# Kernel optimization log

Measured on AMD Instinct MI355X. Metric: run time of the kernel, lower is better.

Reference implementation:

```python
import jax, jax.numpy as jnp
import numpy as np

D_IN = 768
D_OUT = 768
NUM_HEADS = 12
HEAD_DIM = D_OUT // NUM_HEADS


def setup_inputs() -> dict:
    key = jax.random.key(0)
    ks = jax.random.split(key, 9)
    s = 1.0 / np.sqrt(D_IN)
    x = jax.random.normal(ks[0], (8, 1024, D_IN), dtype=jnp.float32)
    Wq = jax.random.uniform(ks[1], (D_IN, D_OUT), jnp.float32, -s, s)
    Wk = jax.random.uniform(ks[2], (D_IN, D_OUT), jnp.float32, -s, s)
    Wv = jax.random.uniform(ks[3], (D_IN, D_OUT), jnp.float32, -s, s)
    Wo = jax.random.uniform(ks[4], (D_OUT, D_OUT), jnp.float32, -s, s)
    bq = jax.random.uniform(ks[5], (D_OUT,), jnp.float32, -s, s)
    bk = jax.random.uniform(ks[6], (D_OUT,), jnp.float32, -s, s)
    bv = jax.random.uniform(ks[7], (D_OUT,), jnp.float32, -s, s)
    bo = jax.random.uniform(ks[8], (D_OUT,), jnp.float32, -s, s)
    return {"x": x, "Wq": Wq, "bq": bq, "Wk": Wk, "bk": bk,
            "Wv": Wv, "bv": bv, "Wo": Wo, "bo": bo}


def reference(x, Wq, bq, Wk, bk, Wv, bv, Wo, bo):
    b, n, _ = x.shape
    # projections -> (b, heads, n, head_dim)
    def split_heads(t):
        return t.reshape(b, n, NUM_HEADS, HEAD_DIM).transpose(0, 2, 1, 3)
    q = split_heads(x @ Wq + bq)
    k = split_heads(x @ Wk + bk)
    v = split_heads(x @ Wv + bv)
    scale = 1.0 / jnp.sqrt(jnp.float32(HEAD_DIM)).astype(x.dtype)
    scores = jnp.einsum('bhqd,bhkd->bhqk', q, k) * scale
    attn = jax.nn.softmax(scores, axis=-1)  # dropout p=0.0 -> identity
    ctx = jnp.einsum('bhqk,bhkd->bhqd', attn, v)
    ctx = ctx.transpose(0, 2, 1, 3).reshape(b, n, D_OUT)
    return ctx @ Wo + bo
```

## Files before the change

### kernel.cpp

```cpp
#include <hip/hip_runtime.h>
#include <math.h>

#define D_MODEL 768
#define NHEAD  12
#define HDIM   64
#define SEQ    1024
#define BATCH  8
#define MTOT   (BATCH*SEQ)
#define QKV_LD 2304

typedef _Float16 f16;
typedef __attribute__((ext_vector_type(2))) __fp16 fp16x2;
typedef __attribute__((ext_vector_type(4))) _Float16 f16x4;
typedef __attribute__((ext_vector_type(8))) _Float16 f16x8;
typedef __attribute__((ext_vector_type(4))) float f32x4;
typedef __attribute__((ext_vector_type(16))) float f32x16;

union PFrag { unsigned u[4]; f16x8 v; };
union PackW { fp16x2 h; unsigned u; };

__device__ inline void gload_lds16(const void* g, void* l) {
    __builtin_amdgcn_global_load_lds(
        (const __attribute__((address_space(1))) void*)g,
        (__attribute__((address_space(3))) void*)l, 16, 0, 0);
}

__global__ __launch_bounds__(256) void cvt_f32_f16(
    const float* __restrict__ in, f16* __restrict__ out, int n8)
{
    const int i = blockIdx.x * 256 + threadIdx.x;
    if (i < n8) {
        const float4 a = *(const float4*)(in + (size_t)i * 8);
        const float4 b = *(const float4*)(in + (size_t)i * 8 + 4);
        f16x8 v;
        v[0] = (f16)a.x; v[1] = (f16)a.y; v[2] = (f16)a.z; v[3] = (f16)a.w;
        v[4] = (f16)b.x; v[5] = (f16)b.y; v[6] = (f16)b.z; v[7] = (f16)b.w;
        *(f16x8*)(out + (size_t)i * 8) = v;
    }
}

__global__ __launch_bounds__(256) void concat_bias(
    const float* __restrict__ bq, const float* __restrict__ bk,
    const float* __restrict__ bv, float* __restrict__ bqkv)
{
    const int i = blockIdx.x * 256 + threadIdx.x;
    if (i < QKV_LD)
        bqkv[i] = (i < 768) ? bq[i] : (i < 1536) ? bk[i - 768] : bv[i - 1536];
}

__global__ __launch_bounds__(256) void transpose_cvt_all(
    const float* __restrict__ Wq, const float* __restrict__ Wk,
    const float* __restrict__ Wv, const float* __restrict__ Wo,
    f16* __restrict__ Wqkv_t, f16* __restrict__ Wo_t)
{
    const int z = blockIdx.z;
    const float* src = (z == 0) ? Wq : (z == 1) ? Wk : (z == 2) ? Wv : Wo;
    f16* dst = (z < 3) ? (Wqkv_t + (size_t)z * 768 * 768) : Wo_t;

    __shared__ f16 tile[64][72];
    const int t  = threadIdx.x;
    const int k0 = blockIdx.y * 64;
    const int n0 = blockIdx.x * 64;
    {
        const int r  = t >> 4;
        const int c4 = (t & 15) * 4;
        #pragma unroll
        for (int u = 0; u < 4; ++u) {
            const int row = r + u * 16;
            const float4 a = *(const float4*)&src[(size_t)(k0 + row) * 768 + n0 + c4];
            tile[row][c4 + 0] = (f16)a.x;
            tile[row][c4 + 1] = (f16)a.y;
            tile[row][c4 + 2] = (f16)a.z;
            tile[row][c4 + 3] = (f16)a.w;
        }
    }
    __syncthreads();
    {
        const int rn = t >> 3;
        const int ck = (t & 7) * 8;
        #pragma unroll
        for (int u = 0; u < 2; ++u) {
            const int n = rn + u * 32;
            f16x8 v;
            #pragma unroll
            for (int q = 0; q < 8; ++q) v[q] = tile[ck + q][n];
            *(f16x8*)&dst[(size_t)(n0 + n) * 768 + k0 + ck] = v;
        }
    }
}

template<typename OUT_T>
__global__ __launch_bounds__(256) void gemm_f16_tn(
    const f16* __restrict__ A, const f16* __restrict__ Bt,
    const float* __restrict__ bias, OUT_T* __restrict__ C,
    int M, int N, int K, int nb)
{
    __shared__ f16 As[128 * 32];
    __shared__ f16 Bs[128 * 32];

    const int t    = threadIdx.x;
    const int l    = t & 63;
    const int w    = t >> 6;
    const int l15  = l & 15;
    const int lg   = l >> 4;
    const int wrow = (w >> 1) * 64;
    const int wcol = (w & 1) * 64;

    const int orig = blockIdx.x;
    const int cpx  = gridDim.x >> 3;
    const int nid  = (orig & 7) * cpx + (orig >> 3);
    const int row0 = (nid / nb) * 128;
    const int col0 = (nid % nb) * 128;

    int src_row[2], src_koff[2], lds_off[2];
    #pragma unroll
    for (int i = 0; i < 2; ++i) {
        const int c = t + 256 * i;
        const int r = c >> 2;
        src_row[i]  = r;
        src_koff[i] = (((c & 3) - (r >> 1)) & 3) * 8;
        lds_off[i]  = c * 16;
    }

    int a_off[4], b_off[4];
    #pragma unroll
    for (int i = 0; i < 4; ++i) {
        const int ra = wrow + i * 16 + l15;
        a_off[i] = ra * 64 + (((lg + (ra >> 1)) & 3) * 16);
        const int rb = wcol + i * 16 + l15;
        b_off[i] = rb * 64 + (((lg + (rb >> 1)) & 3) * 16);
    }

    f32x4 acc[4][4];
    #pragma unroll
    for (int i = 0; i < 4; ++i)
        #pragma unroll
        for (int j = 0; j < 4; ++j)
            acc[i][j] = (f32x4){0.f, 0.f, 0.f, 0.f};

    const f16* Abase = A  + (size_t)row0 * K;
    const f16* Bbase = Bt + (size_t)col0 * K;

    for (int k0 = 0; k0 < K; k0 += 32) {
        #pragma unroll
        for (int i = 0; i < 2; ++i) {
            gload_lds16(Abase + (size_t)src_row[i] * K + k0 + src_koff[i],
                        (char*)As + lds_off[i]);
            gload_lds16(Bbase + (size_t)src_row[i] * K + k0 + src_koff[i],
                        (char*)Bs + lds_off[i]);
        }
        __syncthreads();

        f16x8 af[4], bf[4];
        #pragma unroll
        for (int i = 0; i < 4; ++i) {
            af[i] = *(const f16x8*)((const char*)As + a_off[i]);
            bf[i] = *(const f16x8*)((const char*)Bs + b_off[i]);
        }
        #pragma unroll
        for (int i = 0; i < 4; ++i)
            #pragma unroll
            for (int j = 0; j < 4; ++j)
                acc[i][j] = __builtin_amdgcn_mfma_f32_16x16x32_f16(
                    af[i], bf[j], acc[i][j], 0, 0, 0);
        __syncthreads();
    }

    #pragma unroll
    for (int j = 0; j < 4; ++j) {
        const int col = col0 + wcol + j * 16 + l15;
        const float bj = bias[col];
        #pragma unroll
        for (int i = 0; i < 4; ++i) {
            const int row = row0 + wrow + i * 16 + lg * 4;
            #pragma unroll
            for (int q = 0; q < 4; ++q)
                C[(size_t)(row + q) * N + col] = (OUT_T)(acc[i][j][q] + bj);
        }
    }
}

#define RESCALE_THR 10.0f
#define QMAP(r, hh) (((r) & 3) + 8 * ((r) >> 2) + 4 * (hh))

__global__ __launch_bounds__(256, 3) void attn_f16(
    const f16* __restrict__ QKV, f16* __restrict__ O)
{
    __shared__ f16 KsB[2][64 * 64];
    __shared__ f16 VtB[2][64 * 64];

    const int t   = threadIdx.x;
    const int w   = t >> 6;
    const int l   = t & 63;
    const int l31 = l & 31;
    const int h   = l >> 5;
    const int sl  = (l & 7) << 4;

    const int orig = blockIdx.x;
    const int s    = (orig & 7) * 96 + (orig >> 3);
    const int bh   = s >> 3;
    const int qb   = s & 7;
    const int b  = bh / NHEAD;
    const int hd = bh % NHEAD;
    const int q0 = qb * 128;

    const size_t rowbase = (size_t)b * SEQ;
    const int qcol = hd * HDIM;
    const int kcol = 768 + hd * HDIM;
    const int vcol = 1536 + hd * HDIM;

    const f16 hsc = (f16)(0.125f * 1.4426950408889634f);
    f16x8 qf[4];
    #pragma unroll
    for (int dc = 0; dc < 4; ++dc) {
        f16x8 v = *(const f16x8*)(QKV
            + (rowbase + q0 + w * 32 + l31) * QKV_LD
            + qcol + dc * 16 + h * 8);
        #pragma unroll
        for (int j = 0; j < 8; ++j) v[j] *= hsc;
        qf[dc] = v;
    }

    f32x16 ctx[2];
    #pragma unroll
    for (int dt = 0; dt < 2; ++dt)
        #pragma unroll
        for (int r = 0; r < 16; ++r) ctx[dt][r] = 0.f;
    float mrun = -INFINITY;
    float lrun = 0.f;

    const int cb  = w * 16;
    const int vk0 = (l & 15) * 4;
    const int vd0 = ((l >> 4) + 4 * w) * 4;
    const f16* kptr = QKV + (rowbase + l)   * QKV_LD + kcol + cb;
    const f16* vptr = QKV + (rowbase + vk0) * QKV_LD + vcol + vd0;
    const size_t step = (size_t)64 * QKV_LD;

    f16x8 kr0, kr1;
    f16x4 vr[4];
    kr0 = *(const f16x8*)(kptr);
    kr1 = *(const f16x8*)(kptr + 8);
    #pragma unroll
    for (int i = 0; i < 4; ++i)
        vr[i] = *(const f16x4*)(vptr + (size_t)i * QKV_LD);

    {
        char* Kd = (char*)KsB[0];
        char* Vd = (char*)VtB[0];
        *(f16x8*)(Kd + l * 128 + ((cb * 2)      ^ sl)) = kr0;
        *(f16x8*)(Kd + l * 128 + ((cb * 2 + 16) ^ sl)) = kr1;
        #pragma unroll
        for (int di = 0; di < 4; ++di) {
            f16x4 wt;
            #pragma unroll
            for (int i = 0; i < 4; ++i) wt[i] = vr[i][di];
            *(f16x4*)(Vd + (vd0 + di) * 128
                         + ((vk0 * 2) ^ (((vd0 + di) & 7) << 4))) = wt;
        }
    }
    kr0 = *(const f16x8*)(kptr + step);
    kr1 = *(const f16x8*)(kptr + step + 8);
    #pragma unroll
    for (int i = 0; i < 4; ++i)
        vr[i] = *(const f16x4*)(vptr + step + (size_t)i * QKV_LD);
    __syncthreads();

    for (int kt = 0; kt < SEQ / 64; ++kt) {
        const int p = kt & 1;
        const char* Kp = (const char*)KsB[p];
        const char* Vp = (const char*)VtB[p];

        f32x16 sacc[2];
        __builtin_amdgcn_s_setprio(1);
        #pragma unroll
        for (int kk = 0; kk < 2; ++kk) {
            f32x16 a;
            #pragma unroll
            for (int r = 0; r < 16; ++r) a[r] = 0.f;
            #pragma unroll
            for (int dc = 0; dc < 4; ++dc) {
                const f16x8 ka = *(const f16x8*)(Kp + (kk * 32 + l31) * 128
                                                    + ((dc * 32 + h * 16) ^ sl));
                a = __builtin_amdgcn_mfma_f32_32x32x16_f16(ka, qf[dc], a, 0, 0, 0);
            }
            sacc[kk] = a;
        }
        __builtin_amdgcn_s_setprio(0);

        {
            float tmax = sacc[0][0];
            #pragma unroll
            for (int r = 1; r < 16; ++r) tmax = fmaxf(tmax, sacc[0][r]);
            #pragma unroll
            for (int r = 0; r < 16; ++r) tmax = fmaxf(tmax, sacc[1][r]);
            tmax = fmaxf(tmax, __shfl_xor(tmax, 32));

            if (__any(tmax > mrun + RESCALE_THR)) {
                const float mnew = fmaxf(mrun, tmax);
                const float corr = exp2f(mrun - mnew);
                mrun = mnew;
                lrun *= corr;
                #pragma unroll
                for (int r = 0; r < 16; ++r) {
                    const float cr = __shfl(corr, QMAP(r, h));
                    ctx[0][r] *= cr;
                    ctx[1][r] *= cr;
                }
            }

            float ps = 0.f;
            #pragma unroll
            for (int kk = 0; kk < 2; ++kk)
                #pragma unroll
                for (int r = 0; r < 16; ++r) {
                    const float pe = exp2f(sacc[kk][r] - mrun);
                    ps += pe;
                    sacc[kk][r] = pe;
                }
            ps += __shfl_xor(ps, 32);
            lrun += ps;
        }

        unsigned paw[4][4];
        #pragma unroll
        for (int kk = 0; kk < 2; ++kk) {
            unsigned dw[8];
            #pragma unroll
            for (int i = 0; i < 8; ++i) {
                PackW u;
                u.h = __builtin_amdgcn_cvt_pkrtz(sacc[kk][2 * i], sacc[kk][2 * i + 1]);
                dw[i] = u.u;
            }
            const unsigned t0 = (unsigned)__shfl_xor((int)(h ? dw[0] : dw[2]), 32);
            const unsigned t1 = (unsigned)__shfl_xor((int)(h ? dw[1] : dw[3]), 32);
            const unsigned t2 = (unsigned)__shfl_xor((int)(h ? dw[4] : dw[6]), 32);
            const unsigned t3 = (unsigned)__shfl_xor((int)(h ? dw[5] : dw[7]), 32);
            paw[2 * kk][0]     = h ? t0    : dw[0];
            paw[2 * kk][1]     = h ? t1    : dw[1];
            paw[2 * kk][2]     = h ? dw[2] : t0;
            paw[2 * kk][3]     = h ? dw[3] : t1;
            paw[2 * kk + 1][0] = h ? t2    : dw[4];
            paw[2 * kk + 1][1] = h ? t3    : dw[5];
            paw[2 * kk + 1][2] = h ? dw[6] : t2;
            paw[2 * kk + 1][3] = h ? dw[7] : t3;
        }

        __builtin_amdgcn_s_setprio(1);
        #pragma unroll
        for (int c = 0; c < 4; ++c) {
            PFrag pf;
            pf.u[0] = paw[c][0]; pf.u[1] = paw[c][1];
            pf.u[2] = paw[c][2]; pf.u[3] = paw[c][3];
            #pragma unroll
            for (int dt = 0; dt < 2; ++dt) {
                const f16x8 vb = *(const f16x8*)(Vp + (dt * 32 + l31) * 128
                                                    + ((c * 32 + h * 16) ^ sl));
                ctx[dt] = __builtin_amdgcn_mfma_f32_32x32x16_f16(pf.v, vb, ctx[dt], 0, 0, 0);
            }
        }
        __builtin_amdgcn_s_setprio(0);

        if (kt < SEQ / 64 - 1) {
            char* Kd = (char*)KsB[p ^ 1];
            char* Vd = (char*)VtB[p ^ 1];
            *(f16x8*)(Kd + l * 128 + ((cb * 2)      ^ sl)) = kr0;
            *(f16x8*)(Kd + l * 128 + ((cb * 2 + 16) ^ sl)) = kr1;
            #pragma unroll
            for (int di = 0; di < 4; ++di) {
                f16x4 wt;
                #pragma unroll
                for (int i = 0; i < 4; ++i) wt[i] = vr[i][di];
                *(f16x4*)(Vd + (vd0 + di) * 128
                             + ((vk0 * 2) ^ (((vd0 + di) & 7) << 4))) = wt;
            }
            if (kt < SEQ / 64 - 2) {
                const f16* kp = kptr + (size_t)(kt + 2) * step;
                const f16* vp = vptr + (size_t)(kt + 2) * step;
                kr0 = *(const f16x8*)(kp);
                kr1 = *(const f16x8*)(kp + 8);
                #pragma unroll
                for (int i = 0; i < 4; ++i)
                    vr[i] = *(const f16x4*)(vp + (size_t)i * QKV_LD);
            }
        }
        __syncthreads();
    }

    {
        const float inv = 1.0f / lrun;
        #pragma unroll
        for (int r = 0; r < 16; ++r) {
            const float iv = __shfl(inv, QMAP(r, h));
            const size_t row = rowbase + q0 + w * 32 + QMAP(r, h);
            O[row * D_MODEL + qcol + l31]      = (f16)(ctx[0][r] * iv);
            O[row * D_MODEL + qcol + 32 + l31] = (f16)(ctx[1][r] * iv);
        }
    }
}

extern "C" void kernel_launch(void* const* d_in, const int* in_sizes, int n_in,
                              void* d_out, int out_size, void* d_ws, size_t ws_size,
                              hipStream_t stream) {
    const float* x  = (const float*)d_in[0];
    const float* Wq = (const float*)d_in[1];
    const float* bq = (const float*)d_in[2];
    const float* Wk = (const float*)d_in[3];
    const float* bk = (const float*)d_in[4];
    const float* Wv = (const float*)d_in[5];
    const float* bv = (const float*)d_in[6];
    const float* Wo = (const float*)d_in[7];
    const float* bo = (const float*)d_in[8];
    float* out = (float*)d_out;

    char* ws = (char*)d_ws;
    f16*   QKV     = (f16*)(ws);
    f16*   xh      = (f16*)(ws + 37748736);
    f16*   ctxh    = (f16*)(ws + 37748736 + 12582912);
    f16*   Wqkv_t  = (f16*)(ws + 37748736 + 2 * 12582912);
    f16*   Wo_t    = (f16*)(ws + 37748736 + 2 * 12582912 + 3538944);
    float* bqkv    = (float*)(ws + 37748736 + 2 * 12582912 + 3538944 + 1179648);

    hipLaunchKernelGGL(cvt_f32_f16, dim3(MTOT * D_MODEL / 8 / 256), dim3(256), 0, stream,
                       x, xh, MTOT * D_MODEL / 8);
    hipLaunchKernelGGL(concat_bias, dim3(9), dim3(256), 0, stream, bq, bk, bv, bqkv);
    hipLaunchKernelGGL(transpose_cvt_all, dim3(12, 12, 4), dim3(256), 0, stream,
                       Wq, Wk, Wv, Wo, Wqkv_t, Wo_t);

    hipLaunchKernelGGL((gemm_f16_tn<f16>), dim3((QKV_LD / 128) * (MTOT / 128)), dim3(256), 0, stream,
                       xh, Wqkv_t, bqkv, QKV, MTOT, QKV_LD, D_MODEL, QKV_LD / 128);

    hipLaunchKernelGGL(attn_f16, dim3((SEQ / 128) * BATCH * NHEAD), dim3(256), 0, stream,
                       QKV, ctxh);

    hipLaunchKernelGGL((gemm_f16_tn<float>), dim3((D_MODEL / 128) * (MTOT / 128)), dim3(256), 0, stream,
                       ctxh, Wo_t, bo, out, MTOT, D_MODEL, D_MODEL, D_MODEL / 128);
}
```

Baseline: 139.8 us.

## Split KV sequence across wave pairs in attention and merge partial softmax states

The attention kernel now processes 64 query rows per block instead of 128, doubling the grid. The four waves form two pairs, each pair handling half of the key/value sequence (8 tiles each) with its own single-buffered shared-memory tiles. Partial (max, sum, context) states are merged through shared memory at the end, and occupancy is raised to 4 blocks per CU. Row max and sum reductions are also rewritten as tree reductions. The aim is more parallelism and shorter per-block serial loops, at the cost of an extra merge step, an extra barrier per iteration, and no double buffering.

```diff
diff --git a/kernel.cpp b/kernel.cpp
--- a/kernel.cpp
+++ b/kernel.cpp
@@ -183,38 +183,42 @@
 #define RESCALE_THR 10.0f
 #define QMAP(r, hh) (((r) & 3) + 8 * ((r) >> 2) + 4 * (hh))
 
-__global__ __launch_bounds__(256, 3) void attn_f16(
+__global__ __launch_bounds__(256, 4) void attn_f16(
     const f16* __restrict__ QKV, f16* __restrict__ O)
 {
-    __shared__ f16 KsB[2][64 * 64];
-    __shared__ f16 VtB[2][64 * 64];
+    __shared__ __align__(16) char smem[32768];
 
     const int t   = threadIdx.x;
     const int w   = t >> 6;
     const int l   = t & 63;
     const int l31 = l & 31;
     const int h   = l >> 5;
+    const int g   = w >> 1;
+    const int sh  = w & 1;
     const int sl  = (l & 7) << 4;
 
     const int orig = blockIdx.x;
-    const int s    = (orig & 7) * 96 + (orig >> 3);
-    const int bh   = s >> 3;
-    const int qb   = s & 7;
+    const int s    = (orig & 7) * 192 + (orig >> 3);
+    const int bh   = s >> 4;
+    const int qb   = s & 15;
     const int b  = bh / NHEAD;
     const int hd = bh % NHEAD;
-    const int q0 = qb * 128;
+    const int q0 = qb * 64;
 
     const size_t rowbase = (size_t)b * SEQ;
     const int qcol = hd * HDIM;
     const int kcol = 768 + hd * HDIM;
     const int vcol = 1536 + hd * HDIM;
 
+    char* Ksh = smem + sh * 8192;
+    char* Vsh = smem + 16384 + sh * 8192;
+
     const f16 hsc = (f16)(0.125f * 1.4426950408889634f);
     f16x8 qf[4];
     #pragma unroll
     for (int dc = 0; dc < 4; ++dc) {
         f16x8 v = *(const f16x8*)(QKV
-            + (rowbase + q0 + w * 32 + l31) * QKV_LD
+            + (rowbase + q0 + g * 32 + l31) * QKV_LD
             + qcol + dc * 16 + h * 8);
         #pragma unroll
         for (int j = 0; j < 8; ++j) v[j] *= hsc;
@@ -229,47 +233,40 @@
     float mrun = -INFINITY;
     float lrun = 0.f;
 
-    const int cb  = w * 16;
+    const int kc0 = g * 32;
     const int vk0 = (l & 15) * 4;
-    const int vd0 = ((l >> 4) + 4 * w) * 4;
-    const f16* kptr = QKV + (rowbase + l)   * QKV_LD + kcol + cb;
+    const int vd0 = (l >> 4) * 8 + g * 32;
+    const f16* kptr = QKV + (rowbase + l)   * QKV_LD + kcol + kc0;
     const f16* vptr = QKV + (rowbase + vk0) * QKV_LD + vcol + vd0;
     const size_t step = (size_t)64 * QKV_LD;
-
-    f16x8 kr0, kr1;
-    f16x4 vr[4];
-    kr0 = *(const f16x8*)(kptr);
-    kr1 = *(const f16x8*)(kptr + 8);
-    #pragma unroll
-    for (int i = 0; i < 4; ++i)
-        vr[i] = *(const f16x4*)(vptr + (size_t)i * QKV_LD);
-
-    {
-        char* Kd = (char*)KsB[0];
-        char* Vd = (char*)VtB[0];
-        *(f16x8*)(Kd + l * 128 + ((cb * 2)      ^ sl)) = kr0;
-        *(f16x8*)(Kd + l * 128 + ((cb * 2 + 16) ^ sl)) = kr1;
-        #pragma unroll
-        for (int di = 0; di < 4; ++di) {
-            f16x4 wt;
-            #pragma unroll
-            for (int i = 0; i < 4; ++i) wt[i] = vr[i][di];
-            *(f16x4*)(Vd + (vd0 + di) * 128
-                         + ((vk0 * 2) ^ (((vd0 + di) & 7) << 4))) = wt;
-        }
-    }
-    kr0 = *(const f16x8*)(kptr + step);
-    kr1 = *(const f16x8*)(kptr + step + 8);
-    #pragma unroll
-    for (int i = 0; i < 4; ++i)
-        vr[i] = *(const f16x4*)(vptr + step + (size_t)i * QKV_LD);
+    const size_t tb   = (size_t)(sh * 8) * step;
+
+    f16x8 kr[4], vr[4];
+    #pragma unroll
+    for (int j = 0; j < 4; ++j) {
+        kr[j] = *(const f16x8*)(kptr + tb + j * 8);
+        vr[j] = *(const f16x8*)(vptr + tb + (size_t)j * QKV_LD);
+    }
+
+    #pragma unroll
+    for (int j = 0; j < 4; ++j)
+        *(f16x8*)(Ksh + l * 128 + (((kc0 + j * 8) * 2) ^ sl)) = kr[j];
+    #pragma unroll
+    for (int dj = 0; dj < 8; ++dj) {
+        f16x4 wt;
+        #pragma unroll
+        for (int i = 0; i < 4; ++i) wt[i] = vr[i][dj];
+        *(f16x4*)(Vsh + (vd0 + dj) * 128
+                     + ((vk0 * 2) ^ (((vd0 + dj) & 7) << 4))) = wt;
+    }
+    #pragma unroll
+    for (int j = 0; j < 4; ++j) {
+        kr[j] = *(const f16x8*)(kptr + tb + step + j * 8);
+        vr[j] = *(const f16x8*)(vptr + tb + step + (size_t)j * QKV_LD);
+    }
     __syncthreads();
 
-    for (int kt = 0; kt < SEQ / 64; ++kt) {
-        const int p = kt & 1;
-        const char* Kp = (const char*)KsB[p];
-        const char* Vp = (const char*)VtB[p];
-
+    for (int it = 0; it < 8; ++it) {
         f32x16 sacc[2];
         __builtin_amdgcn_s_setprio(1);
         #pragma unroll
@@ -279,8 +276,8 @@
             for (int r = 0; r < 16; ++r) a[r] = 0.f;
             #pragma unroll
             for (int dc = 0; dc < 4; ++dc) {
-                const f16x8 ka = *(const f16x8*)(Kp + (kk * 32 + l31) * 128
-                                                    + ((dc * 32 + h * 16) ^ sl));
+                const f16x8 ka = *(const f16x8*)(Ksh + (kk * 32 + l31) * 128
+                                                     + ((dc * 32 + h * 16) ^ sl));
                 a = __builtin_amdgcn_mfma_f32_32x32x16_f16(ka, qf[dc], a, 0, 0, 0);
             }
             sacc[kk] = a;
@@ -288,12 +285,16 @@
         __builtin_amdgcn_s_setprio(0);
 
         {
-            float tmax = sacc[0][0];
-            #pragma unroll
-            for (int r = 1; r < 16; ++r) tmax = fmaxf(tmax, sacc[0][r]);
-            #pragma unroll
-            for (int r = 0; r < 16; ++r) tmax = fmaxf(tmax, sacc[1][r]);
-            tmax = fmaxf(tmax, __shfl_xor(tmax, 32));
+            float tm[16];
+            #pragma unroll
+            for (int r = 0; r < 16; ++r)
+                tm[r] = fmaxf(sacc[0][r], sacc[1][r]);
+            #pragma unroll
+            for (int off = 8; off >= 1; off >>= 1)
+                #pragma unroll
+                for (int r = 0; r < 8; ++r)
+                    if (r < off) tm[r] = fmaxf(tm[r], tm[r + off]);
+            float tmax = fmaxf(tm[0], __shfl_xor(tm[0], 32));
 
             if (__any(tmax > mrun + RESCALE_THR)) {
                 const float mnew = fmaxf(mrun, tmax);
@@ -308,17 +309,21 @@
                 }
             }
 
-            float ps = 0.f;
+            float sm[16];
             #pragma unroll
             for (int kk = 0; kk < 2; ++kk)
                 #pragma unroll
-                for (int r = 0; r < 16; ++r) {
-                    const float pe = exp2f(sacc[kk][r] - mrun);
-                    ps += pe;
-                    sacc[kk][r] = pe;
-                }
-            ps += __shfl_xor(ps, 32);
-            lrun += ps;
+                for (int r = 0; r < 16; ++r)
+                    sacc[kk][r] = exp2f(sacc[kk][r] - mrun);
+            #pragma unroll
+            for (int r = 0; r < 16; ++r)
+                sm[r] = sacc[0][r] + sacc[1][r];
+            #pragma unroll
+            for (int off = 8; off >= 1; off >>= 1)
+                #pragma unroll
+                for (int r = 0; r < 8; ++r)
+                    if (r < off) sm[r] += sm[r + off];
+            lrun += sm[0] + __shfl_xor(sm[0], 32);
         }
 
         unsigned paw[4][4];
@@ -353,47 +358,87 @@
             pf.u[2] = paw[c][2]; pf.u[3] = paw[c][3];
             #pragma unroll
             for (int dt = 0; dt < 2; ++dt) {
-                const f16x8 vb = *(const f16x8*)(Vp + (dt * 32 + l31) * 128
-                                                    + ((c * 32 + h * 16) ^ sl));
+                const f16x8 vb = *(const f16x8*)(Vsh + (dt * 32 + l31) * 128
+                                                     + ((c * 32 + h * 16) ^ sl));
                 ctx[dt] = __builtin_amdgcn_mfma_f32_32x32x16_f16(pf.v, vb, ctx[dt], 0, 0, 0);
             }
         }
         __builtin_amdgcn_s_setprio(0);
 
-        if (kt < SEQ / 64 - 1) {
-            char* Kd = (char*)KsB[p ^ 1];
-            char* Vd = (char*)VtB[p ^ 1];
-            *(f16x8*)(Kd + l * 128 + ((cb * 2)      ^ sl)) = kr0;
-            *(f16x8*)(Kd + l * 128 + ((cb * 2 + 16) ^ sl)) = kr1;
-            #pragma unroll
-            for (int di = 0; di < 4; ++di) {
+        __syncthreads();
+
+        if (it < 7) {
+            #pragma unroll
+            for (int j = 0; j < 4; ++j)
+                *(f16x8*)(Ksh + l * 128 + (((kc0 + j * 8) * 2) ^ sl)) = kr[j];
+            #pragma unroll
+            for (int dj = 0; dj < 8; ++dj) {
                 f16x4 wt;
                 #pragma unroll
-                for (int i = 0; i < 4; ++i) wt[i] = vr[i][di];
-                *(f16x4*)(Vd + (vd0 + di) * 128
-                             + ((vk0 * 2) ^ (((vd0 + di) & 7) << 4))) = wt;
-            }
-            if (kt < SEQ / 64 - 2) {
-                const f16* kp = kptr + (size_t)(kt + 2) * step;
-                const f16* vp = vptr + (size_t)(kt + 2) * step;
-                kr0 = *(const f16x8*)(kp);
-                kr1 = *(const f16x8*)(kp + 8);
-                #pragma unroll
-                for (int i = 0; i < 4; ++i)
-                    vr[i] = *(const f16x4*)(vp + (size_t)i * QKV_LD);
+                for (int i = 0; i < 4; ++i) wt[i] = vr[i][dj];
+                *(f16x4*)(Vsh + (vd0 + dj) * 128
+                             + ((vk0 * 2) ^ (((vd0 + dj) & 7) << 4))) = wt;
+            }
+            if (it < 6) {
+                const size_t off = tb + (size_t)(it + 2) * step;
+                #pragma unroll
+                for (int j = 0; j < 4; ++j) {
+                    kr[j] = *(const f16x8*)(kptr + off + j * 8);
+                    vr[j] = *(const f16x8*)(vptr + off + (size_t)j * QKV_LD);
+                }
             }
         }
         __syncthreads();
     }
 
     {
-        const float inv = 1.0f / lrun;
-        #pragma unroll
-        for (int r = 0; r < 16; ++r) {
-            const float iv = __shfl(inv, QMAP(r, h));
-            const size_t row = rowbase + q0 + w * 32 + QMAP(r, h);
-            O[row * D_MODEL + qcol + l31]      = (f16)(ctx[0][r] * iv);
-            O[row * D_MODEL + qcol + 32 + l31] = (f16)(ctx[1][r] * iv);
+        float* cb = (float*)(smem + g * 9216 + l * 144);
+        float2* mlb = (float2*)(smem + 18432);
+        if (sh == 1) {
+            #pragma unroll
+            for (int dt = 0; dt < 2; ++dt)
+                #pragma unroll
+                for (int c = 0; c < 4; ++c) {
+                    f32x4 v;
+                    v[0] = ctx[dt][c * 4 + 0]; v[1] = ctx[dt][c * 4 + 1];
+                    v[2] = ctx[dt][c * 4 + 2]; v[3] = ctx[dt][c * 4 + 3];
+                    *(f32x4*)(cb + dt * 16 + c * 4) = v;
+                }
+            mlb[g * 64 + l] = make_float2(mrun, lrun);
+        }
+        __syncthreads();
+        if (sh == 0) {
+            const float2 ml = mlb[g * 64 + l];
+            const float mN = fmaxf(mrun, ml.x);
+            const float fa = exp2f(mrun - mN);
+            const float fb = exp2f(ml.x - mN);
+            lrun = lrun * fa + ml.y * fb;
+            f32x16 cB[2];
+            #pragma unroll
+            for (int dt = 0; dt < 2; ++dt)
+                #pragma unroll
+                for (int c = 0; c < 4; ++c) {
+                    const f32x4 v = *(const f32x4*)(cb + dt * 16 + c * 4);
+                    cB[dt][c * 4 + 0] = v[0]; cB[dt][c * 4 + 1] = v[1];
+                    cB[dt][c * 4 + 2] = v[2]; cB[dt][c * 4 + 3] = v[3];
+                }
+            #pragma unroll
+            for (int r = 0; r < 16; ++r) {
+                const int src = QMAP(r, h);
+                const float faq = __shfl(fa, src);
+                const float fbq = __shfl(fb, src);
+                ctx[0][r] = ctx[0][r] * faq + cB[0][r] * fbq;
+                ctx[1][r] = ctx[1][r] * faq + cB[1][r] * fbq;
+            }
+
+            const float inv = 1.0f / lrun;
+            #pragma unroll
+            for (int r = 0; r < 16; ++r) {
+                const float iv = __shfl(inv, QMAP(r, h));
+                const size_t row = rowbase + q0 + g * 32 + QMAP(r, h);
+                O[row * D_MODEL + qcol + l31]      = (f16)(ctx[0][r] * iv);
+                O[row * D_MODEL + qcol + 32 + l31] = (f16)(ctx[1][r] * iv);
+            }
         }
     }
 }
@@ -429,7 +474,7 @@
     hipLaunchKernelGGL((gemm_f16_tn<f16>), dim3((QKV_LD / 128) * (MTOT / 128)), dim3(256), 0, stream,
                        xh, Wqkv_t, bqkv, QKV, MTOT, QKV_LD, D_MODEL, QKV_LD / 128);
 
-    hipLaunchKernelGGL(attn_f16, dim3((SEQ / 128) * BATCH * NHEAD), dim3(256), 0, stream,
+    hipLaunchKernelGGL(attn_f16, dim3((SEQ / 64) * BATCH * NHEAD), dim3(256), 0, stream,
                        QKV, ctxh);
 
     hipLaunchKernelGGL((gemm_f16_tn<float>), dim3((D_MODEL / 128) * (MTOT / 128)), dim3(256), 0, stream,
```

Result: slower. 225.7 us (+61.4%).
